# Kernel tuning notes

Hardware: AMD Instinct MI355X
Metric: run time of the kernel (lower is better)

## Reference

```python
import jax, jax.numpy as jnp
from jax import lax
import numpy as np

# GConv2d config (matches init_kwargs)
OUT_TRANSFORMS = 4  # rotations: 0, 90, 180, 270 degrees
STRIDE = 1
PADDING = 1


def setup_inputs() -> dict:
    key = jax.random.key(0)
    k1, k2, k3, k4 = jax.random.split(key, 4)
    B, IC_EFF, H, W = 16, 256, 64, 64   # IC_EFF = in_channels * in_transformations
    OC, K, F = 64, 4, 3                 # out_channels, num_dynamic_kernels, filter_size
    x = jax.random.normal(k1, (B, IC_EFF, H, W), dtype=jnp.float32)
    W_fc = jax.random.normal(k2, (K, IC_EFF), dtype=jnp.float32) * (1.0 / np.sqrt(IC_EFF))
    b_fc = jnp.zeros((K,), dtype=jnp.float32)
    kernel_bank = jax.random.normal(k3, (K, OC, IC_EFF, F, F), dtype=jnp.float32)
    return {"x": x, "W_fc": W_fc, "b_fc": b_fc, "kernel_bank": kernel_bank}


def reference(x, W_fc, b_fc, kernel_bank):
    B, C, H, W = x.shape
    # Dynamic routing: global average pool -> linear -> softmax over kernel bank
    pooled = x.mean(axis=(2, 3))                      # [B, C]
    coeffs = jax.nn.softmax(pooled @ W_fc.T + b_fc, axis=1)  # [B, K]
    # Sample-specific base kernels: mix of kernel bank
    base = jnp.einsum('bk,kocij->bocij', coeffs, kernel_bank)  # [B, oc, C, f, f]
    # P4 orientation expansion: rotate kernel spatially, stack along out-channels
    oriented = jnp.concatenate(
        [jnp.rot90(base, k, axes=(-2, -1)) for k in range(OUT_TRANSFORMS)], axis=1
    )  # [B, 4*oc, C, f, f]
    O, f = oriented.shape[1], oriented.shape[-1]
    # Batched per-sample conv via grouped convolution (one launch instead of B)
    xg = x.reshape(1, B * C, H, W)
    kg = oriented.reshape(B * O, C, f, f)
    out = lax.conv_general_dilated(
        xg, kg,
        window_strides=(STRIDE, STRIDE),
        padding=[(PADDING, PADDING), (PADDING, PADDING)],
        dimension_numbers=('NCHW', 'OIHW', 'NCHW'),
        feature_group_count=B,
    )  # [1, B*O, H', W']
    Ho, Wo = out.shape[-2], out.shape[-1]
    return out.reshape(B, O, Ho, Wo)
```

## Files before the change

### kernel.cpp

```cpp
#include <hip/hip_runtime.h>

#define B_  16
#define C_  256
#define O_  256

typedef short    bf16x8 __attribute__((ext_vector_type(8)));
typedef float    f32x16 __attribute__((ext_vector_type(16)));
typedef unsigned u32x4  __attribute__((ext_vector_type(4)));
typedef unsigned u32x2  __attribute__((ext_vector_type(2)));

#define XROW_SH  1056
#define XBC_SH   (66 * XROW_SH)
#define XT_BYTES ((size_t)B_ * 16 * XBC_SH * 2)

#define WTILE_SH 9216
#define WORP_BYTES ((size_t)B_ * 16 * 4 * WTILE_SH * 2)

#define XBUF_SH  10752

__device__ __forceinline__ unsigned cvtpk(float lo, float hi) {
    unsigned r;
    asm("v_cvt_pk_bf16_f32 %0, %1, %2" : "=v"(r) : "v"(lo), "v"(hi));
    return r;
}

__device__ __forceinline__ void gload16(const void* g, void* l) {
    __builtin_amdgcn_global_load_lds(
        (const __attribute__((address_space(1))) unsigned int*)g,
        (__attribute__((address_space(3))) unsigned int*)l, 16, 0, 0);
}

__global__ __launch_bounds__(256) void xprep_kernel(const float* __restrict__ x,
                                                    short* __restrict__ xT,
                                                    float* __restrict__ pooled4) {
    const int cg = blockIdx.x;
    const int b  = blockIdx.y;
    const int z  = blockIdx.z;
    const int t  = threadIdx.x;
    const int lane = t & 63, wv = t >> 6;
    const int cc = cg >> 1, lh = cg & 1;

    short* xTb = xT + (size_t)(b * 16 + cc) * XBC_SH;
    const float* xb = x + ((size_t)(b * C_ + cg * 8) << 12);

    {
        u32x4 zv = {0, 0, 0, 0};
        if (t < 32) {
            int r   = z * 16 + 1 + (t >> 1);
            int col = (t & 1) ? 65 : 0;
            *(u32x4*)&xTb[r * XROW_SH + lh * 528 + col * 8] = zv;
        }
        if (z == 0 || z == 3) {
            int row = (z == 0) ? 0 : 65;
            if (t < 66) *(u32x4*)&xTb[row * XROW_SH + lh * 528 + t * 8] = zv;
        }
    }

    float s[8] = {0.f, 0.f, 0.f, 0.f, 0.f, 0.f, 0.f, 0.f};
    const int px = lane;
#pragma unroll
    for (int r = 0; r < 4; ++r) {
        const int row = z * 16 + wv * 4 + r;
        const float* src = xb + row * 64 + px;
        float v[8];
#pragma unroll
        for (int i = 0; i < 8; ++i) { v[i] = src[(size_t)i << 12]; s[i] += v[i]; }
        u32x4 d = { cvtpk(v[0], v[1]), cvtpk(v[2], v[3]),
                    cvtpk(v[4], v[5]), cvtpk(v[6], v[7]) };
        *(u32x4*)&xTb[(row + 1) * XROW_SH + lh * 528 + (px + 1) * 8] = d;
    }

#pragma unroll
    for (int i = 0; i < 8; ++i)
#pragma unroll
        for (int off = 32; off; off >>= 1) s[i] += __shfl_xor(s[i], off, 64);

    __shared__ float pr[4][8];
    if (lane == 0) {
#pragma unroll
        for (int i = 0; i < 8; ++i) pr[wv][i] = s[i];
    }
    __syncthreads();
    if (t < 8) {
        float v = pr[0][t] + pr[1][t] + pr[2][t] + pr[3][t];
        pooled4[(z * B_ + b) * C_ + cg * 8 + t] = v * (1.0f / 4096.0f);
    }
}

__global__ __launch_bounds__(256) void mix_kernel(const float* __restrict__ bank,
                                                  const float* __restrict__ pooled4,
                                                  const float* __restrict__ W_fc,
                                                  const float* __restrict__ b_fc,
                                                  short* __restrict__ worp) {
    const int b  = blockIdx.x;
    const int cc = blockIdx.y;
    const int t  = threadIdx.x, lane = t & 63, wid = t >> 6;

    __shared__ float bankL[4 * 64 * 37];
    __shared__ float lg[4];

    {
        float s = 0.f;
#pragma unroll
        for (int q = 0; q < 4; ++q) {
            int c = lane * 4 + q;
            float pv = pooled4[b * C_ + c] + pooled4[(B_ + b) * C_ + c]
                     + pooled4[(2 * B_ + b) * C_ + c] + pooled4[(3 * B_ + b) * C_ + c];
            s += pv * W_fc[wid * C_ + c];
        }
#pragma unroll
        for (int off = 32; off; off >>= 1) s += __shfl_down(s, off, 64);
        if (lane == 0) lg[wid] = s + b_fc[wid];
    }
    __syncthreads();
    float l0 = lg[0], l1 = lg[1], l2 = lg[2], l3 = lg[3];
    float mx = fmaxf(fmaxf(l0, l1), fmaxf(l2, l3));
    float e0 = expf(l0 - mx), e1 = expf(l1 - mx), e2 = expf(l2 - mx), e3 = expf(l3 - mx);
    float inv = 1.f / (e0 + e1 + e2 + e3);
    const float cf0 = e0 * inv, cf1 = e1 * inv, cf2 = e2 * inv, cf3 = e3 * inv;

    const int oq  = t >> 6;
    const int o64 = t & 63;

    for (int sub = 0; sub < 4; ++sub) {
        __syncthreads();
        for (int i = t; i < 9216; i += 256) {
            int run = i / 36, e = i % 36;
            bankL[run * 37 + e] = bank[((size_t)run * C_ + cc * 16 + sub * 4) * 9 + e];
        }
        __syncthreads();

        const int lhs = sub >> 1;
        const float* bp = &bankL[o64 * 37];
#pragma unroll
        for (int ti = 0; ti < 3; ++ti)
#pragma unroll
            for (int tj = 0; tj < 3; ++tj) {
                int si, sj;
                if      (oq == 0) { si = ti;     sj = tj;     }
                else if (oq == 1) { si = tj;     sj = 2 - ti; }
                else if (oq == 2) { si = 2 - ti; sj = 2 - tj; }
                else              { si = 2 - tj; sj = ti;     }
                const int sij = si * 3 + sj;
                float v[4];
#pragma unroll
                for (int c4 = 0; c4 < 4; ++c4) {
                    const float* q = bp + c4 * 9 + sij;
                    v[c4] = cf0 * q[0] + cf1 * q[64 * 37] + cf2 * q[2 * 64 * 37]
                          + cf3 * q[3 * 64 * 37];
                }
                u32x2 d = { cvtpk(v[0], v[1]), cvtpk(v[2], v[3]) };
                size_t base = (((((size_t)(b * 16 + cc) * 4 + oq) * 9 + (ti * 3 + tj)) * 2
                                + lhs) * 64 + o64) * 8 + (sub & 1) * 4;
                *(u32x2*)&worp[base] = d;
            }
    }
}

__global__ __launch_bounds__(256, 2)
void conv_mfma(const short* __restrict__ xT, const short* __restrict__ worp,
               float* __restrict__ out) {
    __shared__ short lds[2 * XBUF_SH + 2 * WTILE_SH];

    const int g    = blockIdx.x;
    const int w    = (g & 7) * 64 + (g >> 3);
    const int oq   = w & 3;
    const int m    = w >> 2;
    const int rowt = m & 7;
    const int b    = m >> 3;
    const int y0   = rowt * 8;

    const int t    = threadIdx.x;
    const int lane = t & 63;
    const int wid  = t >> 6;
    const int l31  = lane & 31;
    const int lh   = lane >> 5;

    const char* xsrcB = (const char*)xT
        + ((size_t)(b * 16) * XBC_SH + (size_t)y0 * XROW_SH) * 2 + lane * 16;
    const char* wsrcB = (const char*)worp
        + (((size_t)(b * 16) * 4) + oq) * (WTILE_SH * 2) + lane * 16;

#define STAGE(ccc, p)                                                           \
    { const char* xs = xsrcB + (size_t)(ccc) * (XBC_SH * 2);                    \
      const char* ws = wsrcB + (size_t)(ccc) * (4 * WTILE_SH * 2);              \
      char* xd = (char*)lds + (p) * (XBUF_SH * 2);                              \
      char* wd = (char*)lds + 2 * (XBUF_SH * 2) + (p) * (WTILE_SH * 2);         \
      for (int u = wid; u < 21; u += 4) gload16(xs + u * 1024, xd + u * 1024);  \
      for (int u = wid; u < 18; u += 4) gload16(ws + u * 1024, wd + u * 1024); }

#define BRD(r, s) (*(const bf16x8*)&xcur[(((r) * 2 + lh) * 66 + (s) + l31) * 8])
#define LOADROW(R, r)                                                           \
    { R[0] = BRD(r, 0);  R[1] = BRD(r, 1);  R[2] = BRD(r, 2);                   \
      R[3] = BRD(r, 32); R[4] = BRD(r, 33); R[5] = BRD(r, 34); }

#define TAPROW(i, RA, RB)                                                       \
    _Pragma("unroll")                                                           \
    for (int j = 0; j < 3; ++j) {                                               \
        const int tap = (i) * 3 + j;                                            \
        const short* wp = wcur + ((tap * 2 + lh) * 64 + l31) * 8;               \
        bf16x8 A0 = *(const bf16x8*)wp;                                         \
        bf16x8 A1 = *(const bf16x8*)(wp + 256);                                 \
        acc0[0] = __builtin_amdgcn_mfma_f32_32x32x16_bf16(A0, RA[j],     acc0[0], 0, 0, 0); \
        acc1[0] = __builtin_amdgcn_mfma_f32_32x32x16_bf16(A1, RA[j],     acc1[0], 0, 0, 0); \
        acc0[1] = __builtin_amdgcn_mfma_f32_32x32x16_bf16(A0, RA[3 + j], acc0[1], 0, 0, 0); \
        acc1[1] = __builtin_amdgcn_mfma_f32_32x32x16_bf16(A1, RA[3 + j], acc1[1], 0, 0, 0); \
        acc0[2] = __builtin_amdgcn_mfma_f32_32x32x16_bf16(A0, RB[j],     acc0[2], 0, 0, 0); \
        acc1[2] = __builtin_amdgcn_mfma_f32_32x32x16_bf16(A1, RB[j],     acc1[2], 0, 0, 0); \
        acc0[3] = __builtin_amdgcn_mfma_f32_32x32x16_bf16(A0, RB[3 + j], acc0[3], 0, 0, 0); \
        acc1[3] = __builtin_amdgcn_mfma_f32_32x32x16_bf16(A1, RB[3 + j], acc1[3], 0, 0, 0); \
    }

#define PHASE_EDGE()                                                            \
    __builtin_amdgcn_sched_barrier(0);                                          \
    __builtin_amdgcn_s_barrier();

    f32x16 acc0[4] = {}, acc1[4] = {};

    STAGE(0, 0);
    __syncthreads();

    for (int cc = 0; cc < 16; ++cc) {
        const int p = cc & 1;
        const short* xcur = lds + p * XBUF_SH;
        const short* wcur = lds + 2 * XBUF_SH + p * WTILE_SH;

        bf16x8 R0[6], R1[6];
        LOADROW(R0, 2 * wid);
        LOADROW(R1, 2 * wid + 1);
        if (cc < 15) STAGE(cc + 1, p ^ 1);
        PHASE_EDGE();
        __builtin_amdgcn_s_setprio(1);
        TAPROW(0, R0, R1)
        __builtin_amdgcn_s_setprio(0);
        LOADROW(R0, 2 * wid + 2);
        PHASE_EDGE();
        __builtin_amdgcn_s_setprio(1);
        TAPROW(1, R1, R0)
        __builtin_amdgcn_s_setprio(0);
        LOADROW(R1, 2 * wid + 3);
        PHASE_EDGE();
        __builtin_amdgcn_s_setprio(1);
        TAPROW(2, R0, R1)
        __builtin_amdgcn_s_setprio(0);
        __syncthreads();
    }
#undef STAGE
#undef BRD
#undef LOADROW
#undef TAPROW
#undef PHASE_EDGE

#pragma unroll
    for (int pf = 0; pf < 4; ++pf) {
        const int yb  = y0 + 2 * wid + (pf >> 1);
        const int xcb = 32 * (pf & 1) + l31;
#pragma unroll
        for (int r = 0; r < 16; ++r) {
            const int orow = (r & 3) + 8 * (r >> 2) + 4 * lh;
            const int o0   = oq * 64 + orow;
            __builtin_nontemporal_store(acc0[pf][r],
                &out[((size_t)(b * O_ + o0)      << 12) + yb * 64 + xcb]);
            __builtin_nontemporal_store(acc1[pf][r],
                &out[((size_t)(b * O_ + o0 + 32) << 12) + yb * 64 + xcb]);
        }
    }
}

extern "C" void kernel_launch(void* const* d_in, const int* in_sizes, int n_in,
                              void* d_out, int out_size, void* d_ws, size_t ws_size,
                              hipStream_t stream) {
    const float* x    = (const float*)d_in[0];
    const float* W_fc = (const float*)d_in[1];
    const float* b_fc = (const float*)d_in[2];
    const float* bank = (const float*)d_in[3];
    float* out = (float*)d_out;

    short* xTb     = (short*)d_ws;
    short* worp    = (short*)((char*)d_ws + XT_BYTES);
    float* pooled4 = (float*)((char*)d_ws + XT_BYTES + WORP_BYTES);

    xprep_kernel<<<dim3(32, 16, 4), 256, 0, stream>>>(x, xTb, pooled4);
    mix_kernel<<<dim3(B_, 16), 256, 0, stream>>>(bank, pooled4, W_fc, b_fc, worp);
    conv_mfma<<<512, 256, 0, stream>>>(xTb, worp, out);
}
```

Before: 111.5 us.

## Restructure kernel mixing grid for bank reuse and drop intra-loop barriers in conv

The mix kernel now runs one block per (channel chunk, 16-output group). Each block loads its bank slice into LDS once and reuses it for all 16 batch samples, where before the bank was reloaded for every sample. Each thread computes the softmax coefficients, mixes 8 channels and writes 16-byte packed stores. In the conv kernel, the per-phase s_barrier/sched_barrier edges are removed and a third row register set is preloaded, so taps run without cross-wave synchronisation. The cost is higher register pressure, and the coefficient computation is now a serial 256-step loop per thread.

```diff
diff --git a/kernel.cpp b/kernel.cpp
--- a/kernel.cpp
+++ b/kernel.cpp
@@ -7,7 +7,6 @@
 typedef short    bf16x8 __attribute__((ext_vector_type(8)));
 typedef float    f32x16 __attribute__((ext_vector_type(16)));
 typedef unsigned u32x4  __attribute__((ext_vector_type(4)));
-typedef unsigned u32x2  __attribute__((ext_vector_type(2)));
 
 #define XROW_SH  1056
 #define XBC_SH   (66 * XROW_SH)
@@ -92,68 +91,82 @@
                                                   const float* __restrict__ W_fc,
                                                   const float* __restrict__ b_fc,
                                                   short* __restrict__ worp) {
-    const int b  = blockIdx.x;
-    const int cc = blockIdx.y;
-    const int t  = threadIdx.x, lane = t & 63, wid = t >> 6;
-
-    __shared__ float bankL[4 * 64 * 37];
-    __shared__ float lg[4];
-
-    {
-        float s = 0.f;
-#pragma unroll
-        for (int q = 0; q < 4; ++q) {
-            int c = lane * 4 + q;
+    const int cc = blockIdx.x;
+    const int og = blockIdx.y;
+    const int t  = threadIdx.x;
+
+    __shared__ float bankL[4 * 16 * 16 * 10];
+    __shared__ float cfs[16][4];
+
+    for (int i = t; i < 4 * 16 * 16 * 9; i += 256) {
+        int k  = i / 2304, r = i % 2304;
+        int oc = r / 144,  r2 = r % 144;
+        int c  = r2 / 9,   tap = r2 % 9;
+        bankL[((k * 16 + oc) * 16 + c) * 10 + tap] =
+            bank[(((size_t)k * 64 + og * 16 + oc) * C_ + cc * 16 + c) * 9 + tap];
+    }
+    if (t < 64) {
+        int b = t >> 2, k = t & 3;
+        float s = b_fc[k];
+        for (int c = 0; c < C_; ++c) {
             float pv = pooled4[b * C_ + c] + pooled4[(B_ + b) * C_ + c]
                      + pooled4[(2 * B_ + b) * C_ + c] + pooled4[(3 * B_ + b) * C_ + c];
-            s += pv * W_fc[wid * C_ + c];
-        }
-#pragma unroll
-        for (int off = 32; off; off >>= 1) s += __shfl_down(s, off, 64);
-        if (lane == 0) lg[wid] = s + b_fc[wid];
-    }
-    __syncthreads();
-    float l0 = lg[0], l1 = lg[1], l2 = lg[2], l3 = lg[3];
-    float mx = fmaxf(fmaxf(l0, l1), fmaxf(l2, l3));
-    float e0 = expf(l0 - mx), e1 = expf(l1 - mx), e2 = expf(l2 - mx), e3 = expf(l3 - mx);
-    float inv = 1.f / (e0 + e1 + e2 + e3);
-    const float cf0 = e0 * inv, cf1 = e1 * inv, cf2 = e2 * inv, cf3 = e3 * inv;
-
-    const int oq  = t >> 6;
-    const int o64 = t & 63;
-
-    for (int sub = 0; sub < 4; ++sub) {
-        __syncthreads();
-        for (int i = t; i < 9216; i += 256) {
-            int run = i / 36, e = i % 36;
-            bankL[run * 37 + e] = bank[((size_t)run * C_ + cc * 16 + sub * 4) * 9 + e];
-        }
-        __syncthreads();
-
-        const int lhs = sub >> 1;
-        const float* bp = &bankL[o64 * 37];
-#pragma unroll
-        for (int ti = 0; ti < 3; ++ti)
-#pragma unroll
-            for (int tj = 0; tj < 3; ++tj) {
+            s += pv * W_fc[k * C_ + c];
+        }
+        cfs[b][k] = s;
+    }
+    __syncthreads();
+    if (t < 16) {
+        float l0 = cfs[t][0], l1 = cfs[t][1], l2 = cfs[t][2], l3 = cfs[t][3];
+        float mx = fmaxf(fmaxf(l0, l1), fmaxf(l2, l3));
+        float e0 = expf(l0 - mx), e1 = expf(l1 - mx);
+        float e2 = expf(l2 - mx), e3 = expf(l3 - mx);
+        float inv = 1.f / (e0 + e1 + e2 + e3);
+        cfs[t][0] = e0 * inv; cfs[t][1] = e1 * inv;
+        cfs[t][2] = e2 * inv; cfs[t][3] = e3 * inv;
+    }
+    __syncthreads();
+
+    const int oc_l = t & 15;
+    const int lhs  = (t >> 4) & 1;
+    const int bg   = t >> 5;
+    const int o64  = og * 16 + oc_l;
+
+#pragma unroll
+    for (int bb = 0; bb < 2; ++bb) {
+        const int b = bg * 2 + bb;
+        const float c0 = cfs[b][0], c1 = cfs[b][1], c2 = cfs[b][2], c3 = cfs[b][3];
+        float mixed[8][9];
+#pragma unroll
+        for (int ci = 0; ci < 8; ++ci) {
+            const float* p0 = &bankL[((0 * 16 + oc_l) * 16 + lhs * 8 + ci) * 10];
+            const float* p1 = p0 + 16 * 16 * 10;
+            const float* p2 = p0 + 2 * 16 * 16 * 10;
+            const float* p3 = p0 + 3 * 16 * 16 * 10;
+#pragma unroll
+            for (int tp = 0; tp < 9; ++tp)
+                mixed[ci][tp] = c0 * p0[tp] + c1 * p1[tp] + c2 * p2[tp] + c3 * p3[tp];
+        }
+#pragma unroll
+        for (int oq = 0; oq < 4; ++oq) {
+#pragma unroll
+            for (int td = 0; td < 9; ++td) {
+                const int ti = td / 3, tj = td % 3;
                 int si, sj;
                 if      (oq == 0) { si = ti;     sj = tj;     }
                 else if (oq == 1) { si = tj;     sj = 2 - ti; }
                 else if (oq == 2) { si = 2 - ti; sj = 2 - tj; }
                 else              { si = 2 - tj; sj = ti;     }
-                const int sij = si * 3 + sj;
-                float v[4];
-#pragma unroll
-                for (int c4 = 0; c4 < 4; ++c4) {
-                    const float* q = bp + c4 * 9 + sij;
-                    v[c4] = cf0 * q[0] + cf1 * q[64 * 37] + cf2 * q[2 * 64 * 37]
-                          + cf3 * q[3 * 64 * 37];
-                }
-                u32x2 d = { cvtpk(v[0], v[1]), cvtpk(v[2], v[3]) };
-                size_t base = (((((size_t)(b * 16 + cc) * 4 + oq) * 9 + (ti * 3 + tj)) * 2
-                                + lhs) * 64 + o64) * 8 + (sub & 1) * 4;
-                *(u32x2*)&worp[base] = d;
+                const int ts = si * 3 + sj;
+                u32x4 d = { cvtpk(mixed[0][ts], mixed[1][ts]),
+                            cvtpk(mixed[2][ts], mixed[3][ts]),
+                            cvtpk(mixed[4][ts], mixed[5][ts]),
+                            cvtpk(mixed[6][ts], mixed[7][ts]) };
+                size_t base = ((((((size_t)b * 16 + cc) * 4 + oq) * 9 + td) * 2
+                                + lhs) * 64 + o64) * 8;
+                *(u32x4*)&worp[base] = d;
             }
+        }
     }
 }
 
@@ -211,10 +224,6 @@
         acc1[3] = __builtin_amdgcn_mfma_f32_32x32x16_bf16(A1, RB[3 + j], acc1[3], 0, 0, 0); \
     }
 
-#define PHASE_EDGE()                                                            \
-    __builtin_amdgcn_sched_barrier(0);                                          \
-    __builtin_amdgcn_s_barrier();
-
     f32x16 acc0[4] = {}, acc1[4] = {};
 
     STAGE(0, 0);
@@ -225,23 +234,18 @@
         const short* xcur = lds + p * XBUF_SH;
         const short* wcur = lds + 2 * XBUF_SH + p * WTILE_SH;
 
-        bf16x8 R0[6], R1[6];
-        LOADROW(R0, 2 * wid);
-        LOADROW(R1, 2 * wid + 1);
+        bf16x8 Ra[6], Rb[6], Rc[6];
+        LOADROW(Ra, 2 * wid);
+        LOADROW(Rb, 2 * wid + 1);
+        LOADROW(Rc, 2 * wid + 2);
         if (cc < 15) STAGE(cc + 1, p ^ 1);
-        PHASE_EDGE();
         __builtin_amdgcn_s_setprio(1);
-        TAPROW(0, R0, R1)
+        TAPROW(0, Ra, Rb)
         __builtin_amdgcn_s_setprio(0);
-        LOADROW(R0, 2 * wid + 2);
-        PHASE_EDGE();
+        LOADROW(Ra, 2 * wid + 3);
         __builtin_amdgcn_s_setprio(1);
-        TAPROW(1, R1, R0)
-        __builtin_amdgcn_s_setprio(0);
-        LOADROW(R1, 2 * wid + 3);
-        PHASE_EDGE();
-        __builtin_amdgcn_s_setprio(1);
-        TAPROW(2, R0, R1)
+        TAPROW(1, Rb, Rc)
+        TAPROW(2, Rc, Ra)
         __builtin_amdgcn_s_setprio(0);
         __syncthreads();
     }
@@ -249,7 +253,6 @@
 #undef BRD
 #undef LOADROW
 #undef TAPROW
-#undef PHASE_EDGE
 
 #pragma unroll
     for (int pf = 0; pf < 4; ++pf) {
@@ -281,6 +284,6 @@
     float* pooled4 = (float*)((char*)d_ws + XT_BYTES + WORP_BYTES);
 
     xprep_kernel<<<dim3(32, 16, 4), 256, 0, stream>>>(x, xTb, pooled4);
-    mix_kernel<<<dim3(B_, 16), 256, 0, stream>>>(bank, pooled4, W_fc, b_fc, worp);
+    mix_kernel<<<dim3(16, 4), 256, 0, stream>>>(bank, pooled4, W_fc, b_fc, worp);
     conv_mfma<<<512, 256, 0, stream>>>(xTb, worp, out);
 }
```

Result: slower. 123.3 us (+10.5%).
